# Optimization experiments

Measured on AMD Instinct MI355X. Metric: run time of the kernel, lower is better.

## Reference

```python
import jax, jax.numpy as jnp
import numpy as np

N_NODES = 100000
N_EDGES = 3200000
IN_DIM = 256
HID_DIM = 64
OUT_DIM = 64


def setup_inputs() -> dict:
    key = jax.random.key(0)
    k1, k2, k3, k4, k5, k6 = jax.random.split(key, 6)
    x = jax.random.normal(k1, (N_NODES, IN_DIM), dtype=jnp.float32)
    edge_index = jax.random.randint(k2, (2, N_EDGES), 0, N_NODES, dtype=jnp.int32)
    # Glorot-style init for the two GCNConv layers (PyG default: glorot weight, zero bias)
    W1 = jax.random.normal(k3, (IN_DIM, HID_DIM), dtype=jnp.float32) * (1.0 / np.sqrt(IN_DIM))
    b1 = jnp.zeros((HID_DIM,), dtype=jnp.float32)
    W2 = jax.random.normal(k4, (HID_DIM, OUT_DIM), dtype=jnp.float32) * (1.0 / np.sqrt(HID_DIM))
    b2 = jnp.zeros((OUT_DIM,), dtype=jnp.float32)
    return {"x": x, "edge_index": edge_index, "W1": W1, "b1": b1, "W2": W2, "b2": b2}


def _gcn_conv(x, src, dst, deg_inv_sqrt, W, b, n):
    # PyG GCNConv: h = x W; out_i = sum_j norm_ij * h_j + b, with symmetric norm
    h = x @ W                                   # (n, d_out) small GEMM
    norm = deg_inv_sqrt[src] * deg_inv_sqrt[dst]  # (E+n,)
    msg = norm[:, None] * h[src]                # gather (E+n, d_out)
    agg = jax.ops.segment_sum(msg, dst, num_segments=n)  # scatter-add
    return agg + b


def reference(x, edge_index, W1, b1, W2, b2):
    n = x.shape[0]
    loops = jnp.arange(n, dtype=edge_index.dtype)
    src = jnp.concatenate([edge_index[0], loops])
    dst = jnp.concatenate([edge_index[1], loops])
    # degree on destination (col) with added self-loops, weight 1.0
    deg = jax.ops.segment_sum(jnp.ones_like(dst, dtype=x.dtype), dst, num_segments=n)
    deg_inv_sqrt = jnp.where(deg > 0, jax.lax.rsqrt(deg), 0.0)
    h = jax.nn.relu(_gcn_conv(x, src, dst, deg_inv_sqrt, W1, b1, n))
    return _gcn_conv(h, src, dst, deg_inv_sqrt, W2, b2, n)
```

## Files before the change

kernel.cpp:

```cpp
#include <hip/hip_runtime.h>
#include <cstdint>
#include <cstddef>


#define BIN_SHIFT 7
#define BIN_NODES 128
#define MAX_BINS 1024
#define SUP_SHIFT 11
#define FINE_PER_SUP 16
#define NSUP_MAX 64
#define SCAP 56
#define SRC_BITS 17
#define SRC_MASK ((1 << SRC_BITS) - 1)

typedef unsigned short ushort_t;

typedef __attribute__((ext_vector_type(8))) short bf16x8;
typedef __attribute__((ext_vector_type(4))) float f32x4;

union FragB {
  uint4 u;
  bf16x8 b;
};

__device__ __forceinline__ float4 bfq2f4(uint2 p) {
  float4 r;
  r.x = __uint_as_float(p.x << 16);
  r.y = __uint_as_float(p.x & 0xFFFF0000u);
  r.z = __uint_as_float(p.y << 16);
  r.w = __uint_as_float(p.y & 0xFFFF0000u);
  return r;
}
__device__ __forceinline__ unsigned f2bf(float f) {
  unsigned u = __float_as_uint(f);
  return (u + 0x7FFFu + ((u >> 16) & 1u)) >> 16;
}
__device__ __forceinline__ uint2 f42bfq(float4 f) {
  uint2 r;
  r.x = f2bf(f.x) | (f2bf(f.y) << 16);
  r.y = f2bf(f.z) | (f2bf(f.w) << 16);
  return r;
}

__global__ void zero_int(int* __restrict__ p, int n) {
  int i = blockIdx.x * blockDim.x + threadIdx.x;
  if (i < n) p[i] = 0;
}

__global__ __launch_bounds__(256) void bin_count(const int* __restrict__ dst, int E, int nbins,
                                                 int* __restrict__ binCnt) {
  __shared__ int h[MAX_BINS];
  for (int i = threadIdx.x; i < nbins; i += 256) h[i] = 0;
  __syncthreads();
  int stride = gridDim.x * 256;
  for (int e = blockIdx.x * 256 + threadIdx.x; e < E; e += stride)
    atomicAdd(&h[dst[e] >> BIN_SHIFT], 1);
  __syncthreads();
  for (int i = threadIdx.x; i < nbins; i += 256)
    if (h[i]) atomicAdd(&binCnt[i], h[i]);
}

__global__ __launch_bounds__(256) void bin_scan(const int* __restrict__ binCnt, int nbins, int E,
                                                int* __restrict__ binStart,
                                                int* __restrict__ binCursor,
                                                int* __restrict__ supCursor) {
  __shared__ int s[256];
  int t = threadIdx.x;
  int c[4];
  int sum = 0;
#pragma unroll
  for (int i = 0; i < 4; i++) {
    int idx = t * 4 + i;
    c[i] = (idx < nbins) ? binCnt[idx] : 0;
    sum += c[i];
  }
  int v = sum;
  s[t] = v;
  __syncthreads();
  for (int d = 1; d < 256; d <<= 1) {
    int add = (t >= d) ? s[t - d] : 0;
    __syncthreads();
    s[t] += add;
    __syncthreads();
  }
  int run = s[t] - v;
#pragma unroll
  for (int i = 0; i < 4; i++) {
    int idx = t * 4 + i;
    if (idx < nbins) {
      binStart[idx] = run;
      binCursor[idx] = run;
      if ((idx & (FINE_PER_SUP - 1)) == 0) supCursor[idx >> 4] = run;
      run += c[i];
    }
  }
  if (t == 0) binStart[nbins] = E;
}

__global__ __launch_bounds__(256) void super_fill(const int* __restrict__ src,
                                                  const int* __restrict__ dst, int E, int nsup,
                                                  int* __restrict__ supCursor,
                                                  unsigned* __restrict__ supbuf) {
  __shared__ unsigned stage[NSUP_MAX * SCAP];
  __shared__ int lcnt[NSUP_MAX], lbase[NSUP_MAX], lscan[NSUP_MAX + 1];
  const int tid = threadIdx.x;
  const int t0 = blockIdx.x * 2048;
  const int t1 = min(E, t0 + 2048);

  int dv[8], sv[8];
#pragma unroll
  for (int i = 0; i < 8; i++) {
    int e = t0 + i * 256 + tid;
    if (e < t1) {
      dv[i] = dst[e];
      sv[i] = src[e];
    }
  }
  if (tid < nsup) lcnt[tid] = 0;
  __syncthreads();
#pragma unroll
  for (int i = 0; i < 8; i++) {
    int e = t0 + i * 256 + tid;
    if (e < t1) {
      int d = dv[i];
      int sb = d >> SUP_SHIFT;
      unsigned v = ((unsigned)(d & ((1 << SUP_SHIFT) - 1)) << SRC_BITS) | (unsigned)sv[i];
      int idx = atomicAdd(&lcnt[sb], 1);
      if (idx < SCAP)
        stage[sb * SCAP + idx] = v;
      else {
        int g = atomicAdd(&supCursor[sb], 1);
        supbuf[g] = v;
      }
    }
  }
  __syncthreads();
  if (tid < nsup) {
    int c = min(lcnt[tid], SCAP);
    lcnt[tid] = c;
    lbase[tid] = c ? atomicAdd(&supCursor[tid], c) : 0;
  }
  __syncthreads();
  if (tid < 64) {
    int vv = (tid < nsup) ? lcnt[tid] : 0;
    int ss = vv;
#pragma unroll
    for (int d = 1; d < 64; d <<= 1) {
      int u = __shfl_up(ss, d);
      if (tid >= d) ss += u;
    }
    lscan[tid + 1] = ss;
    if (tid == 0) lscan[0] = 0;
  }
  __syncthreads();
  int total = lscan[nsup];
  for (int j = tid; j < total; j += 256) {
    int lo = 0, hi = nsup;
    while (hi - lo > 1) {
      int mid = (lo + hi) >> 1;
      if (lscan[mid] <= j)
        lo = mid;
      else
        hi = mid;
    }
    int off = j - lscan[lo];
    supbuf[lbase[lo] + off] = stage[lo * SCAP + off];
  }
}

__global__ __launch_bounds__(256) void fine_fill(const unsigned* __restrict__ supbuf,
                                                 const int* __restrict__ binStart, int nbins,
                                                 int* __restrict__ binCursor,
                                                 unsigned* __restrict__ binbuf) {
  __shared__ int lcnt[FINE_PER_SUP], lbase[FINE_PER_SUP];
  int sb = blockIdx.x >> 3, p = blockIdx.x & 7;
  int seg0 = binStart[sb << 4];
  int seg1 = binStart[min((sb + 1) << 4, nbins)];
  int part = (seg1 - seg0 + 7) >> 3;
  int c0 = seg0 + p * part;
  int c1 = min(seg1, c0 + part);
  if (threadIdx.x < FINE_PER_SUP) lcnt[threadIdx.x] = 0;
  __syncthreads();
  for (int i = c0 + threadIdx.x; i < c1; i += 256) atomicAdd(&lcnt[supbuf[i] >> 24], 1);
  __syncthreads();
  if (threadIdx.x < FINE_PER_SUP) {
    int c = lcnt[threadIdx.x];
    lbase[threadIdx.x] = c ? atomicAdd(&binCursor[(sb << 4) + threadIdx.x], c) : 0;
    lcnt[threadIdx.x] = 0;
  }
  __syncthreads();
  for (int i = c0 + threadIdx.x; i < c1; i += 256) {
    unsigned v = supbuf[i];
    unsigned dls = v >> SRC_BITS;
    int f = dls >> BIN_SHIFT;
    unsigned vf = ((dls & (BIN_NODES - 1)) << SRC_BITS) | (v & SRC_MASK);
    int idx = lbase[f] + atomicAdd(&lcnt[f], 1);
    binbuf[idx] = vf;
  }
}

__global__ __launch_bounds__(256) void bin_csr(const unsigned* __restrict__ binbuf,
                                               const int* __restrict__ binStart, int N, int E,
                                               int* __restrict__ rowptr, int* __restrict__ col,
                                               float* __restrict__ dis) {
  __shared__ int cnt[BIN_NODES];
  __shared__ int cur[BIN_NODES];
  __shared__ int pref[BIN_NODES];
  int b = blockIdx.x, t = threadIdx.x;
  int nodeBase = b << BIN_SHIFT;
  if (t < BIN_NODES) cnt[t] = 0;
  __syncthreads();
  int s0 = binStart[b], s1 = binStart[b + 1];
  for (int i = s0 + t; i < s1; i += 256) atomicAdd(&cnt[binbuf[i] >> SRC_BITS], 1);
  __syncthreads();
  int c = 0;
  if (t < BIN_NODES) {
    int node = nodeBase + t;
    if (node < N) {
      c = cnt[t];
      dis[node] = rsqrtf((float)(c + 1));
    }
    pref[t] = c;
  }
  __syncthreads();
  for (int d = 1; d < BIN_NODES; d <<= 1) {
    int add = (t < BIN_NODES && t >= d) ? pref[t - d] : 0;
    __syncthreads();
    if (t < BIN_NODES) pref[t] += add;
    __syncthreads();
  }
  if (t < BIN_NODES) {
    int node = nodeBase + t;
    if (node < N) {
      int ex = s0 + pref[t] - c;
      rowptr[node] = ex;
      cur[t] = ex;
    }
  }
  if (b == 0 && t == 255) rowptr[N] = E;
  __syncthreads();
  for (int i = s0 + t; i < s1; i += 256) {
    unsigned v = binbuf[i];
    int slot = atomicAdd(&cur[v >> SRC_BITS], 1);
    col[slot] = v & SRC_MASK;
  }
}

__global__ __launch_bounds__(256) void wsplit(const float* __restrict__ W1,
                                              const float* __restrict__ W2,
                                              ushort_t* __restrict__ wt1,
                                              ushort_t* __restrict__ wt2) {
  int i = blockIdx.x * 256 + threadIdx.x;
  const float* W;
  ushort_t* wt;
  int K, idx;
  if (i < 256 * 64) {
    W = W1; wt = wt1; K = 256; idx = i;
  } else if (i < 256 * 64 + 64 * 64) {
    W = W2; wt = wt2; K = 64; idx = i - 256 * 64;
  } else
    return;
  int n = idx & 63, k = idx >> 6;
  float f = W[k * 64 + n];
  unsigned u = __float_as_uint(f);
  unsigned hb = u & 0xFFFF0000u;
  float lo = f - __uint_as_float(hb);
  wt[(size_t)n * K + k] = (ushort_t)(u >> 16);
  wt[(size_t)64 * K + (size_t)n * K + k] = (ushort_t)(__float_as_uint(lo) >> 16);
}

__device__ __forceinline__ void split8u(uint4 a, uint4 b, uint4& xh, uint4& xl) {
  unsigned ua[8] = {a.x, a.y, a.z, a.w, b.x, b.y, b.z, b.w};
  unsigned hw[4], lw[4];
#pragma unroll
  for (int p = 0; p < 4; p++) {
    unsigned u0 = ua[2 * p], u1 = ua[2 * p + 1];
    unsigned h0 = u0 & 0xFFFF0000u, h1 = u1 & 0xFFFF0000u;
    float l0 = __uint_as_float(u0) - __uint_as_float(h0);
    float l1 = __uint_as_float(u1) - __uint_as_float(h1);
    hw[p] = (u0 >> 16) | h1;
    lw[p] = (__float_as_uint(l0) >> 16) | (__float_as_uint(l1) & 0xFFFF0000u);
  }
  xh = make_uint4(hw[0], hw[1], hw[2], hw[3]);
  xl = make_uint4(lw[0], lw[1], lw[2], lw[3]);
}

__global__ __launch_bounds__(256, 2) void gemm1_mfma(const float* __restrict__ A,
                                                     const ushort_t* __restrict__ Wt,
                                                     uint2* __restrict__ Cb, int M) {
  constexpr int K = 256;
  __shared__ uint4 xtile[2][4][512];
  const int lane = threadIdx.x & 63;
  const int wv = threadIdx.x >> 6;
  const int l15 = lane & 15;
  const int lq = lane >> 4;
  const int m0 = blockIdx.x * 256 + wv * 64;

  const ushort_t* __restrict__ Wlo = Wt + (size_t)64 * K;

  f32x4 acc[4][4];
#pragma unroll
  for (int a = 0; a < 4; a++)
#pragma unroll
    for (int b = 0; b < 4; b++) acc[a][b] = (f32x4){0.f, 0.f, 0.f, 0.f};

  auto stage_tile = [&](int kt, int buf) {
#pragma unroll
    for (int c = 0; c < 8; c++) {
      int s = c * 64 + lane;
      int r = s >> 3;
      int c4 = (s & 7) ^ (r & 7);
      int nd = m0 + r;
      if (nd >= M) nd = M - 1;
      const float* gp = A + (size_t)nd * K + kt * 32 + c4 * 4;
      __builtin_amdgcn_global_load_lds(
          (const __attribute__((address_space(1))) void*)gp,
          (__attribute__((address_space(3))) void*)&xtile[buf][wv][c * 64], 16, 0, 0);
    }
  };

  stage_tile(0, 0);
  stage_tile(1, 1);
  __builtin_amdgcn_sched_barrier(0);

#pragma unroll
  for (int j = 0; j < 8; j++) {
    FragB w[8];
    {
      const int kb = j * 32 + lq * 8;
#pragma unroll
      for (int nt = 0; nt < 4; nt++) {
        w[nt].u = *(const uint4*)(Wt + (size_t)(nt * 16 + l15) * K + kb);
        w[4 + nt].u = *(const uint4*)(Wlo + (size_t)(nt * 16 + l15) * K + kb);
      }
    }
    __builtin_amdgcn_sched_barrier(0);
    if (j < 7)
      asm volatile("s_waitcnt vmcnt(16)" ::: "memory");
    else
      asm volatile("s_waitcnt vmcnt(8)" ::: "memory");
    __builtin_amdgcn_sched_barrier(0);
    uint4 xa[4][2];
#pragma unroll
    for (int mt = 0; mt < 4; mt++) {
      int mr = mt * 16 + l15;
#pragma unroll
      for (int hh = 0; hh < 2; hh++) {
        int c4 = (lq * 2 + hh) ^ (mr & 7);
        xa[mt][hh] = *(const uint4*)&xtile[j & 1][wv][mr * 8 + c4];
      }
    }
    __builtin_amdgcn_sched_barrier(0);
    asm volatile("s_waitcnt lgkmcnt(0)" ::: "memory");
    __builtin_amdgcn_sched_barrier(0);
    if (j + 2 < 8) stage_tile(j + 2, j & 1);
    __builtin_amdgcn_sched_barrier(0);
#pragma unroll
    for (int mt = 0; mt < 4; mt++) {
      FragB xh, xl;
      split8u(xa[mt][0], xa[mt][1], xh.u, xl.u);
#pragma unroll
      for (int nt = 0; nt < 4; nt++) {
        acc[mt][nt] = __builtin_amdgcn_mfma_f32_16x16x32_bf16(w[nt].b, xh.b, acc[mt][nt], 0, 0, 0);
        acc[mt][nt] = __builtin_amdgcn_mfma_f32_16x16x32_bf16(w[nt].b, xl.b, acc[mt][nt], 0, 0, 0);
      }
#pragma unroll
      for (int nt = 0; nt < 4; nt++) {
        acc[mt][nt] =
            __builtin_amdgcn_mfma_f32_16x16x32_bf16(w[4 + nt].b, xh.b, acc[mt][nt], 0, 0, 0);
      }
    }
  }

#pragma unroll
  for (int mt = 0; mt < 4; mt++) {
    int node = m0 + mt * 16 + l15;
    if (node < M) {
      uint2* cp = Cb + (size_t)node * 16 + lq;
#pragma unroll
      for (int nt = 0; nt < 4; nt++) {
        float4 o = make_float4(acc[mt][nt][0], acc[mt][nt][1], acc[mt][nt][2], acc[mt][nt][3]);
        cp[nt * 4] = f42bfq(o);
      }
    }
  }
}

__global__ __launch_bounds__(256, 3) void gemm2_mfma(const ushort_t* __restrict__ Av,
                                                     const ushort_t* __restrict__ Wt,
                                                     uint2* __restrict__ Cb, int M) {
  constexpr int K = 64;
  constexpr int NT = K / 32;
  const int lane = threadIdx.x & 63;
  const int wv = threadIdx.x >> 6;
  const int l15 = lane & 15;
  const int lq = lane >> 4;
  const int m0 = blockIdx.x * 128 + wv * 32;

  const ushort_t* __restrict__ Wlo = Wt + (size_t)64 * K;

  f32x4 acc[2][4];
#pragma unroll
  for (int a = 0; a < 2; a++)
#pragma unroll
    for (int b = 0; b < 4; b++) acc[a][b] = (f32x4){0.f, 0.f, 0.f, 0.f};

  int node[2], ncl[2];
#pragma unroll
  for (int mt = 0; mt < 2; mt++) {
    node[mt] = m0 + mt * 16 + l15;
    ncl[mt] = node[mt] < M ? node[mt] : (M - 1);
  }

  FragB xa[NT][2], wh[NT][4], wl[NT][4];
#pragma unroll
  for (int t = 0; t < NT; t++)
#pragma unroll
    for (int mt = 0; mt < 2; mt++)
      xa[t][mt].u = *(const uint4*)(Av + (size_t)ncl[mt] * K + t * 32 + lq * 8);
#pragma unroll
  for (int t = 0; t < NT; t++)
#pragma unroll
    for (int nt = 0; nt < 4; nt++) {
      wh[t][nt].u = *(const uint4*)(Wt + (size_t)(nt * 16 + l15) * K + t * 32 + lq * 8);
      wl[t][nt].u = *(const uint4*)(Wlo + (size_t)(nt * 16 + l15) * K + t * 32 + lq * 8);
    }
#pragma unroll
  for (int t = 0; t < NT; t++)
#pragma unroll
    for (int mt = 0; mt < 2; mt++)
#pragma unroll
      for (int nt = 0; nt < 4; nt++) {
        acc[mt][nt] =
            __builtin_amdgcn_mfma_f32_16x16x32_bf16(wh[t][nt].b, xa[t][mt].b, acc[mt][nt], 0, 0, 0);
        acc[mt][nt] =
            __builtin_amdgcn_mfma_f32_16x16x32_bf16(wl[t][nt].b, xa[t][mt].b, acc[mt][nt], 0, 0, 0);
      }

#pragma unroll
  for (int mt = 0; mt < 2; mt++) {
    if (node[mt] < M) {
      uint2* cp = Cb + (size_t)node[mt] * 16 + lq;
#pragma unroll
      for (int nt = 0; nt < 4; nt++) {
        float4 o = make_float4(acc[mt][nt][0], acc[mt][nt][1], acc[mt][nt][2], acc[mt][nt][3]);
        cp[nt * 4] = f42bfq(o);
      }
    }
  }
}

template <bool OUTBF>
__global__ __launch_bounds__(256) void agg_kernel(
    const uint2* __restrict__ h, const int* __restrict__ rowptr, const int* __restrict__ col,
    const float* __restrict__ dis, const float* __restrict__ bias, void* __restrict__ outv,
    int N, int relu) {
  int wid = (blockIdx.x * blockDim.x + threadIdx.x) >> 6;
  if (wid >= N) return;
  int lane = threadIdx.x & 63;
  int sub = lane & 15;
  int quarter = lane >> 4;

  int start = rowptr[wid], end = rowptr[wid + 1];
  float di = dis[wid];

  float4 a0 = make_float4(0.f, 0.f, 0.f, 0.f), a1 = a0, a2 = a0, a3 = a0;
  {
    float4 self = bfq2f4(h[(size_t)wid * 16 + sub]);
    if (quarter == 0) {
      a0.x = di * self.x;
      a0.y = di * self.y;
      a0.z = di * self.z;
      a0.w = di * self.w;
    }
  }

  for (int base = start; base < end; base += 64) {
    int e = base + lane;
    int sj = 0;
    float wj = 0.f;
    if (e < end) {
      sj = col[e];
      wj = dis[sj];
    }
    int cnt = end - base;
    if (cnt > 64) cnt = 64;
    int rounds = (cnt + 3) >> 2;

    uint2 g0, g1, g2, g3;
    float w0, w1, w2, w3;
#define ISSUE(gi, G, W)                                              \
  do {                                                               \
    int _i = (4 * (gi) + quarter) & 63;                              \
    int _s = __shfl(sj, _i);                                         \
    float _w = __shfl(wj, _i);                                       \
    if ((gi) < rounds) {                                             \
      G = h[(size_t)_s * 16 + sub];                                  \
      W = _w;                                                        \
    } else {                                                         \
      G = make_uint2(0u, 0u);                                        \
      W = 0.f;                                                       \
    }                                                                \
  } while (0)

    ISSUE(0, g0, w0);
    ISSUE(1, g1, w1);
    ISSUE(2, g2, w2);
    ISSUE(3, g3, w3);
    int rounds4 = (rounds + 3) & ~3;
    for (int t0 = 0; t0 < rounds4; t0 += 4) {
      {
        float4 gf = bfq2f4(g0);
        a0.x += w0 * gf.x; a0.y += w0 * gf.y; a0.z += w0 * gf.z; a0.w += w0 * gf.w;
      }
      ISSUE(t0 + 4, g0, w0);
      {
        float4 gf = bfq2f4(g1);
        a1.x += w1 * gf.x; a1.y += w1 * gf.y; a1.z += w1 * gf.z; a1.w += w1 * gf.w;
      }
      ISSUE(t0 + 5, g1, w1);
      {
        float4 gf = bfq2f4(g2);
        a2.x += w2 * gf.x; a2.y += w2 * gf.y; a2.z += w2 * gf.z; a2.w += w2 * gf.w;
      }
      ISSUE(t0 + 6, g2, w2);
      {
        float4 gf = bfq2f4(g3);
        a3.x += w3 * gf.x; a3.y += w3 * gf.y; a3.z += w3 * gf.z; a3.w += w3 * gf.w;
      }
      ISSUE(t0 + 7, g3, w3);
    }
#undef ISSUE
  }

  float sx = (a0.x + a1.x) + (a2.x + a3.x);
  float sy = (a0.y + a1.y) + (a2.y + a3.y);
  float sz = (a0.z + a1.z) + (a2.z + a3.z);
  float sw = (a0.w + a1.w) + (a2.w + a3.w);
  sx += __shfl_down(sx, 32); sy += __shfl_down(sy, 32);
  sz += __shfl_down(sz, 32); sw += __shfl_down(sw, 32);
  sx += __shfl_down(sx, 16); sy += __shfl_down(sy, 16);
  sz += __shfl_down(sz, 16); sw += __shfl_down(sw, 16);
  if (quarter == 0) {
    float4 bv = ((const float4*)bias)[sub];
    float4 o = make_float4(di * sx + bv.x, di * sy + bv.y, di * sz + bv.z, di * sw + bv.w);
    if (relu) {
      o.x = fmaxf(o.x, 0.f);
      o.y = fmaxf(o.y, 0.f);
      o.z = fmaxf(o.z, 0.f);
      o.w = fmaxf(o.w, 0.f);
    }
    if (OUTBF)
      ((uint2*)outv)[(size_t)wid * 16 + sub] = f42bfq(o);
    else
      ((float4*)outv)[(size_t)wid * 16 + sub] = o;
  }
}

extern "C" void kernel_launch(void* const* d_in, const int* in_sizes, int n_in,
                              void* d_out, int out_size, void* d_ws, size_t ws_size,
                              hipStream_t stream) {
  const float* x = (const float*)d_in[0];
  const int* ei = (const int*)d_in[1];
  const float* W1 = (const float*)d_in[2];
  const float* b1 = (const float*)d_in[3];
  const float* W2 = (const float*)d_in[4];
  const float* b2 = (const float*)d_in[5];

  const int IN = 256;
  const int E = in_sizes[1] / 2;
  const int N = in_sizes[0] / IN;
  const int* src = ei;
  const int* dst = ei + E;
  const int nbins = (N + BIN_NODES - 1) >> BIN_SHIFT;
  const int nsup = (N + (1 << SUP_SHIFT) - 1) >> SUP_SHIFT;

  char* ws = (char*)d_ws;
  size_t off = 0;
  auto alloc = [&](size_t bytes) -> void* {
    void* p = ws + off;
    off += (bytes + 255) & ~(size_t)255;
    return p;
  };
  int* rowptr = (int*)alloc((size_t)(N + 1) * 4);
  float* dis = (float*)alloc((size_t)N * 4);
  int* binCnt = (int*)alloc(MAX_BINS * 4);
  int* binStart = (int*)alloc((MAX_BINS + 1) * 4);
  int* binCursor = (int*)alloc(MAX_BINS * 4);
  int* supCursor = (int*)alloc(NSUP_MAX * 4);
  int* col = (int*)alloc((size_t)E * 4);
  unsigned* supbuf = (unsigned*)col;
  uint2* out1 = (uint2*)alloc((size_t)N * 64 * 2);
  size_t big = ((size_t)E * 4 > (size_t)N * 128) ? (size_t)E * 4 : (size_t)N * 128;
  unsigned* binbuf = (unsigned*)alloc(big);
  uint2* h = (uint2*)binbuf;
  ushort_t* wt1 = (ushort_t*)alloc((size_t)2 * 64 * 256 * 2);
  ushort_t* wt2 = (ushort_t*)alloc((size_t)2 * 64 * 64 * 2);
  float* outf = (float*)d_out;

  zero_int<<<(nbins + 255) / 256, 256, 0, stream>>>(binCnt, nbins);
  bin_count<<<1024, 256, 0, stream>>>(dst, E, nbins, binCnt);
  bin_scan<<<1, 256, 0, stream>>>(binCnt, nbins, E, binStart, binCursor, supCursor);
  super_fill<<<(E + 2047) / 2048, 256, 0, stream>>>(src, dst, E, nsup, supCursor, supbuf);
  fine_fill<<<nsup * 8, 256, 0, stream>>>(supbuf, binStart, nbins, binCursor, binbuf);
  bin_csr<<<nbins, 256, 0, stream>>>(binbuf, binStart, N, E, rowptr, col, dis);
  wsplit<<<(256 * 64 + 64 * 64 + 255) / 256, 256, 0, stream>>>(W1, W2, wt1, wt2);

  gemm1_mfma<<<(N + 255) / 256, 256, 0, stream>>>(x, wt1, h, N);
  agg_kernel<true><<<(N + 3) / 4, 256, 0, stream>>>(h, rowptr, col, dis, b1, out1, N, 1);
  gemm2_mfma<<<(N + 127) / 128, 256, 0, stream>>>((const ushort_t*)out1, wt2, h, N);
  agg_kernel<false><<<(N + 3) / 4, 256, 0, stream>>>(h, rowptr, col, dis, b2, outf, N, 0);
}
```

Measured before the change: 453.6 us.

## Stage split weights in swizzled LDS for both GEMMs and fuse zeroing into prep

```diff
diff --git a/kernel.cpp b/kernel.cpp
--- a/kernel.cpp
+++ b/kernel.cpp
@@ -42,215 +42,13 @@
   return r;
 }
 
-__global__ void zero_int(int* __restrict__ p, int n) {
-  int i = blockIdx.x * blockDim.x + threadIdx.x;
-  if (i < n) p[i] = 0;
-}
-
-__global__ __launch_bounds__(256) void bin_count(const int* __restrict__ dst, int E, int nbins,
-                                                 int* __restrict__ binCnt) {
-  __shared__ int h[MAX_BINS];
-  for (int i = threadIdx.x; i < nbins; i += 256) h[i] = 0;
-  __syncthreads();
-  int stride = gridDim.x * 256;
-  for (int e = blockIdx.x * 256 + threadIdx.x; e < E; e += stride)
-    atomicAdd(&h[dst[e] >> BIN_SHIFT], 1);
-  __syncthreads();
-  for (int i = threadIdx.x; i < nbins; i += 256)
-    if (h[i]) atomicAdd(&binCnt[i], h[i]);
-}
-
-__global__ __launch_bounds__(256) void bin_scan(const int* __restrict__ binCnt, int nbins, int E,
-                                                int* __restrict__ binStart,
-                                                int* __restrict__ binCursor,
-                                                int* __restrict__ supCursor) {
-  __shared__ int s[256];
-  int t = threadIdx.x;
-  int c[4];
-  int sum = 0;
-#pragma unroll
-  for (int i = 0; i < 4; i++) {
-    int idx = t * 4 + i;
-    c[i] = (idx < nbins) ? binCnt[idx] : 0;
-    sum += c[i];
-  }
-  int v = sum;
-  s[t] = v;
-  __syncthreads();
-  for (int d = 1; d < 256; d <<= 1) {
-    int add = (t >= d) ? s[t - d] : 0;
-    __syncthreads();
-    s[t] += add;
-    __syncthreads();
-  }
-  int run = s[t] - v;
-#pragma unroll
-  for (int i = 0; i < 4; i++) {
-    int idx = t * 4 + i;
-    if (idx < nbins) {
-      binStart[idx] = run;
-      binCursor[idx] = run;
-      if ((idx & (FINE_PER_SUP - 1)) == 0) supCursor[idx >> 4] = run;
-      run += c[i];
-    }
-  }
-  if (t == 0) binStart[nbins] = E;
-}
-
-__global__ __launch_bounds__(256) void super_fill(const int* __restrict__ src,
-                                                  const int* __restrict__ dst, int E, int nsup,
-                                                  int* __restrict__ supCursor,
-                                                  unsigned* __restrict__ supbuf) {
-  __shared__ unsigned stage[NSUP_MAX * SCAP];
-  __shared__ int lcnt[NSUP_MAX], lbase[NSUP_MAX], lscan[NSUP_MAX + 1];
-  const int tid = threadIdx.x;
-  const int t0 = blockIdx.x * 2048;
-  const int t1 = min(E, t0 + 2048);
-
-  int dv[8], sv[8];
-#pragma unroll
-  for (int i = 0; i < 8; i++) {
-    int e = t0 + i * 256 + tid;
-    if (e < t1) {
-      dv[i] = dst[e];
-      sv[i] = src[e];
-    }
-  }
-  if (tid < nsup) lcnt[tid] = 0;
-  __syncthreads();
-#pragma unroll
-  for (int i = 0; i < 8; i++) {
-    int e = t0 + i * 256 + tid;
-    if (e < t1) {
-      int d = dv[i];
-      int sb = d >> SUP_SHIFT;
-      unsigned v = ((unsigned)(d & ((1 << SUP_SHIFT) - 1)) << SRC_BITS) | (unsigned)sv[i];
-      int idx = atomicAdd(&lcnt[sb], 1);
-      if (idx < SCAP)
-        stage[sb * SCAP + idx] = v;
-      else {
-        int g = atomicAdd(&supCursor[sb], 1);
-        supbuf[g] = v;
-      }
-    }
-  }
-  __syncthreads();
-  if (tid < nsup) {
-    int c = min(lcnt[tid], SCAP);
-    lcnt[tid] = c;
-    lbase[tid] = c ? atomicAdd(&supCursor[tid], c) : 0;
-  }
-  __syncthreads();
-  if (tid < 64) {
-    int vv = (tid < nsup) ? lcnt[tid] : 0;
-    int ss = vv;
-#pragma unroll
-    for (int d = 1; d < 64; d <<= 1) {
-      int u = __shfl_up(ss, d);
-      if (tid >= d) ss += u;
-    }
-    lscan[tid + 1] = ss;
-    if (tid == 0) lscan[0] = 0;
-  }
-  __syncthreads();
-  int total = lscan[nsup];
-  for (int j = tid; j < total; j += 256) {
-    int lo = 0, hi = nsup;
-    while (hi - lo > 1) {
-      int mid = (lo + hi) >> 1;
-      if (lscan[mid] <= j)
-        lo = mid;
-      else
-        hi = mid;
-    }
-    int off = j - lscan[lo];
-    supbuf[lbase[lo] + off] = stage[lo * SCAP + off];
-  }
-}
-
-__global__ __launch_bounds__(256) void fine_fill(const unsigned* __restrict__ supbuf,
-                                                 const int* __restrict__ binStart, int nbins,
-                                                 int* __restrict__ binCursor,
-                                                 unsigned* __restrict__ binbuf) {
-  __shared__ int lcnt[FINE_PER_SUP], lbase[FINE_PER_SUP];
-  int sb = blockIdx.x >> 3, p = blockIdx.x & 7;
-  int seg0 = binStart[sb << 4];
-  int seg1 = binStart[min((sb + 1) << 4, nbins)];
-  int part = (seg1 - seg0 + 7) >> 3;
-  int c0 = seg0 + p * part;
-  int c1 = min(seg1, c0 + part);
-  if (threadIdx.x < FINE_PER_SUP) lcnt[threadIdx.x] = 0;
-  __syncthreads();
-  for (int i = c0 + threadIdx.x; i < c1; i += 256) atomicAdd(&lcnt[supbuf[i] >> 24], 1);
-  __syncthreads();
-  if (threadIdx.x < FINE_PER_SUP) {
-    int c = lcnt[threadIdx.x];
-    lbase[threadIdx.x] = c ? atomicAdd(&binCursor[(sb << 4) + threadIdx.x], c) : 0;
-    lcnt[threadIdx.x] = 0;
-  }
-  __syncthreads();
-  for (int i = c0 + threadIdx.x; i < c1; i += 256) {
-    unsigned v = supbuf[i];
-    unsigned dls = v >> SRC_BITS;
-    int f = dls >> BIN_SHIFT;
-    unsigned vf = ((dls & (BIN_NODES - 1)) << SRC_BITS) | (v & SRC_MASK);
-    int idx = lbase[f] + atomicAdd(&lcnt[f], 1);
-    binbuf[idx] = vf;
-  }
-}
-
-__global__ __launch_bounds__(256) void bin_csr(const unsigned* __restrict__ binbuf,
-                                               const int* __restrict__ binStart, int N, int E,
-                                               int* __restrict__ rowptr, int* __restrict__ col,
-                                               float* __restrict__ dis) {
-  __shared__ int cnt[BIN_NODES];
-  __shared__ int cur[BIN_NODES];
-  __shared__ int pref[BIN_NODES];
-  int b = blockIdx.x, t = threadIdx.x;
-  int nodeBase = b << BIN_SHIFT;
-  if (t < BIN_NODES) cnt[t] = 0;
-  __syncthreads();
-  int s0 = binStart[b], s1 = binStart[b + 1];
-  for (int i = s0 + t; i < s1; i += 256) atomicAdd(&cnt[binbuf[i] >> SRC_BITS], 1);
-  __syncthreads();
-  int c = 0;
-  if (t < BIN_NODES) {
-    int node = nodeBase + t;
-    if (node < N) {
-      c = cnt[t];
-      dis[node] = rsqrtf((float)(c + 1));
-    }
-    pref[t] = c;
-  }
-  __syncthreads();
-  for (int d = 1; d < BIN_NODES; d <<= 1) {
-    int add = (t < BIN_NODES && t >= d) ? pref[t - d] : 0;
-    __syncthreads();
-    if (t < BIN_NODES) pref[t] += add;
-    __syncthreads();
-  }
-  if (t < BIN_NODES) {
-    int node = nodeBase + t;
-    if (node < N) {
-      int ex = s0 + pref[t] - c;
-      rowptr[node] = ex;
-      cur[t] = ex;
-    }
-  }
-  if (b == 0 && t == 255) rowptr[N] = E;
-  __syncthreads();
-  for (int i = s0 + t; i < s1; i += 256) {
-    unsigned v = binbuf[i];
-    int slot = atomicAdd(&cur[v >> SRC_BITS], 1);
-    col[slot] = v & SRC_MASK;
-  }
-}
-
-__global__ __launch_bounds__(256) void wsplit(const float* __restrict__ W1,
-                                              const float* __restrict__ W2,
-                                              ushort_t* __restrict__ wt1,
-                                              ushort_t* __restrict__ wt2) {
+__global__ __launch_bounds__(256) void prep(const float* __restrict__ W1,
+                                            const float* __restrict__ W2,
+                                            ushort_t* __restrict__ wt1,
+                                            ushort_t* __restrict__ wt2,
+                                            int* __restrict__ binCnt, int nbins) {
   int i = blockIdx.x * 256 + threadIdx.x;
+  if (i < nbins) binCnt[i] = 0;
   const float* W;
   ushort_t* wt;
   int K, idx;
@@ -269,6 +67,205 @@
   wt[(size_t)64 * K + (size_t)n * K + k] = (ushort_t)(__float_as_uint(lo) >> 16);
 }
 
+__global__ __launch_bounds__(256) void bin_count(const int* __restrict__ dst, int E, int nbins,
+                                                 int* __restrict__ binCnt) {
+  __shared__ int h[MAX_BINS];
+  for (int i = threadIdx.x; i < nbins; i += 256) h[i] = 0;
+  __syncthreads();
+  int stride = gridDim.x * 256;
+  for (int e = blockIdx.x * 256 + threadIdx.x; e < E; e += stride)
+    atomicAdd(&h[dst[e] >> BIN_SHIFT], 1);
+  __syncthreads();
+  for (int i = threadIdx.x; i < nbins; i += 256)
+    if (h[i]) atomicAdd(&binCnt[i], h[i]);
+}
+
+__global__ __launch_bounds__(256) void bin_scan(const int* __restrict__ binCnt, int nbins, int E,
+                                                int* __restrict__ binStart,
+                                                int* __restrict__ binCursor,
+                                                int* __restrict__ supCursor) {
+  __shared__ int s[256];
+  int t = threadIdx.x;
+  int c[4];
+  int sum = 0;
+#pragma unroll
+  for (int i = 0; i < 4; i++) {
+    int idx = t * 4 + i;
+    c[i] = (idx < nbins) ? binCnt[idx] : 0;
+    sum += c[i];
+  }
+  int v = sum;
+  s[t] = v;
+  __syncthreads();
+  for (int d = 1; d < 256; d <<= 1) {
+    int add = (t >= d) ? s[t - d] : 0;
+    __syncthreads();
+    s[t] += add;
+    __syncthreads();
+  }
+  int run = s[t] - v;
+#pragma unroll
+  for (int i = 0; i < 4; i++) {
+    int idx = t * 4 + i;
+    if (idx < nbins) {
+      binStart[idx] = run;
+      binCursor[idx] = run;
+      if ((idx & (FINE_PER_SUP - 1)) == 0) supCursor[idx >> 4] = run;
+      run += c[i];
+    }
+  }
+  if (t == 0) binStart[nbins] = E;
+}
+
+__global__ __launch_bounds__(256) void super_fill(const int* __restrict__ src,
+                                                  const int* __restrict__ dst, int E, int nsup,
+                                                  int* __restrict__ supCursor,
+                                                  unsigned* __restrict__ supbuf) {
+  __shared__ unsigned stage[NSUP_MAX * SCAP];
+  __shared__ int lcnt[NSUP_MAX], lbase[NSUP_MAX], lscan[NSUP_MAX + 1];
+  const int tid = threadIdx.x;
+  const int t0 = blockIdx.x * 2048;
+  const int t1 = min(E, t0 + 2048);
+
+  int dv[8], sv[8];
+#pragma unroll
+  for (int i = 0; i < 8; i++) {
+    int e = t0 + i * 256 + tid;
+    if (e < t1) {
+      dv[i] = dst[e];
+      sv[i] = src[e];
+    }
+  }
+  if (tid < nsup) lcnt[tid] = 0;
+  __syncthreads();
+#pragma unroll
+  for (int i = 0; i < 8; i++) {
+    int e = t0 + i * 256 + tid;
+    if (e < t1) {
+      int d = dv[i];
+      int sb = d >> SUP_SHIFT;
+      unsigned v = ((unsigned)(d & ((1 << SUP_SHIFT) - 1)) << SRC_BITS) | (unsigned)sv[i];
+      int idx = atomicAdd(&lcnt[sb], 1);
+      if (idx < SCAP)
+        stage[sb * SCAP + idx] = v;
+      else {
+        int g = atomicAdd(&supCursor[sb], 1);
+        supbuf[g] = v;
+      }
+    }
+  }
+  __syncthreads();
+  if (tid < nsup) {
+    int c = min(lcnt[tid], SCAP);
+    lcnt[tid] = c;
+    lbase[tid] = c ? atomicAdd(&supCursor[tid], c) : 0;
+  }
+  __syncthreads();
+  if (tid < 64) {
+    int vv = (tid < nsup) ? lcnt[tid] : 0;
+    int ss = vv;
+#pragma unroll
+    for (int d = 1; d < 64; d <<= 1) {
+      int u = __shfl_up(ss, d);
+      if (tid >= d) ss += u;
+    }
+    lscan[tid + 1] = ss;
+    if (tid == 0) lscan[0] = 0;
+  }
+  __syncthreads();
+  int total = lscan[nsup];
+  for (int j = tid; j < total; j += 256) {
+    int lo = 0, hi = nsup;
+    while (hi - lo > 1) {
+      int mid = (lo + hi) >> 1;
+      if (lscan[mid] <= j)
+        lo = mid;
+      else
+        hi = mid;
+    }
+    int off = j - lscan[lo];
+    supbuf[lbase[lo] + off] = stage[lo * SCAP + off];
+  }
+}
+
+__global__ __launch_bounds__(256) void fine_fill(const unsigned* __restrict__ supbuf,
+                                                 const int* __restrict__ binStart, int nbins,
+                                                 int* __restrict__ binCursor,
+                                                 unsigned* __restrict__ binbuf) {
+  __shared__ int lcnt[FINE_PER_SUP], lbase[FINE_PER_SUP];
+  int sb = blockIdx.x >> 3, p = blockIdx.x & 7;
+  int seg0 = binStart[sb << 4];
+  int seg1 = binStart[min((sb + 1) << 4, nbins)];
+  int part = (seg1 - seg0 + 7) >> 3;
+  int c0 = seg0 + p * part;
+  int c1 = min(seg1, c0 + part);
+  if (threadIdx.x < FINE_PER_SUP) lcnt[threadIdx.x] = 0;
+  __syncthreads();
+  for (int i = c0 + threadIdx.x; i < c1; i += 256) atomicAdd(&lcnt[supbuf[i] >> 24], 1);
+  __syncthreads();
+  if (threadIdx.x < FINE_PER_SUP) {
+    int c = lcnt[threadIdx.x];
+    lbase[threadIdx.x] = c ? atomicAdd(&binCursor[(sb << 4) + threadIdx.x], c) : 0;
+    lcnt[threadIdx.x] = 0;
+  }
+  __syncthreads();
+  for (int i = c0 + threadIdx.x; i < c1; i += 256) {
+    unsigned v = supbuf[i];
+    unsigned dls = v >> SRC_BITS;
+    int f = dls >> BIN_SHIFT;
+    unsigned vf = ((dls & (BIN_NODES - 1)) << SRC_BITS) | (v & SRC_MASK);
+    int idx = lbase[f] + atomicAdd(&lcnt[f], 1);
+    binbuf[idx] = vf;
+  }
+}
+
+__global__ __launch_bounds__(256) void bin_csr(const unsigned* __restrict__ binbuf,
+                                               const int* __restrict__ binStart, int N, int E,
+                                               int* __restrict__ rowptr, int* __restrict__ col,
+                                               float* __restrict__ dis) {
+  __shared__ int cnt[BIN_NODES];
+  __shared__ int cur[BIN_NODES];
+  __shared__ int pref[BIN_NODES];
+  int b = blockIdx.x, t = threadIdx.x;
+  int nodeBase = b << BIN_SHIFT;
+  if (t < BIN_NODES) cnt[t] = 0;
+  __syncthreads();
+  int s0 = binStart[b], s1 = binStart[b + 1];
+  for (int i = s0 + t; i < s1; i += 256) atomicAdd(&cnt[binbuf[i] >> SRC_BITS], 1);
+  __syncthreads();
+  int c = 0;
+  if (t < BIN_NODES) {
+    int node = nodeBase + t;
+    if (node < N) {
+      c = cnt[t];
+      dis[node] = rsqrtf((float)(c + 1));
+    }
+    pref[t] = c;
+  }
+  __syncthreads();
+  for (int d = 1; d < BIN_NODES; d <<= 1) {
+    int add = (t < BIN_NODES && t >= d) ? pref[t - d] : 0;
+    __syncthreads();
+    if (t < BIN_NODES) pref[t] += add;
+    __syncthreads();
+  }
+  if (t < BIN_NODES) {
+    int node = nodeBase + t;
+    if (node < N) {
+      int ex = s0 + pref[t] - c;
+      rowptr[node] = ex;
+      cur[t] = ex;
+    }
+  }
+  if (b == 0 && t == 255) rowptr[N] = E;
+  __syncthreads();
+  for (int i = s0 + t; i < s1; i += 256) {
+    unsigned v = binbuf[i];
+    int slot = atomicAdd(&cur[v >> SRC_BITS], 1);
+    col[slot] = v & SRC_MASK;
+  }
+}
+
 __device__ __forceinline__ void split8u(uint4 a, uint4 b, uint4& xh, uint4& xl) {
   unsigned ua[8] = {a.x, a.y, a.z, a.w, b.x, b.y, b.z, b.w};
   unsigned hw[4], lw[4];
@@ -285,18 +282,27 @@
   xl = make_uint4(lw[0], lw[1], lw[2], lw[3]);
 }
 
-__global__ __launch_bounds__(256, 2) void gemm1_mfma(const float* __restrict__ A,
+__global__ __launch_bounds__(256, 1) void gemm1_mfma(const float* __restrict__ A,
                                                      const ushort_t* __restrict__ Wt,
                                                      uint2* __restrict__ Cb, int M) {
   constexpr int K = 256;
   __shared__ uint4 xtile[2][4][512];
+  __shared__ uint4 wlds[4096];
   const int lane = threadIdx.x & 63;
   const int wv = threadIdx.x >> 6;
   const int l15 = lane & 15;
   const int lq = lane >> 4;
   const int m0 = blockIdx.x * 256 + wv * 64;
 
-  const ushort_t* __restrict__ Wlo = Wt + (size_t)64 * K;
+  {
+    const uint4* wg = (const uint4*)Wt;
+    for (int i = threadIdx.x; i < 4096; i += 256) {
+      int row = (i >> 5) & 63;
+      int k = i & 31;
+      wlds[(i & ~31) | (k ^ (row & 7))] = wg[i];
+    }
+  }
+  __syncthreads();
 
   f32x4 acc[4][4];
 #pragma unroll
@@ -326,19 +332,18 @@
 #pragma unroll
   for (int j = 0; j < 8; j++) {
     FragB w[8];
-    {
-      const int kb = j * 32 + lq * 8;
-#pragma unroll
-      for (int nt = 0; nt < 4; nt++) {
-        w[nt].u = *(const uint4*)(Wt + (size_t)(nt * 16 + l15) * K + kb);
-        w[4 + nt].u = *(const uint4*)(Wlo + (size_t)(nt * 16 + l15) * K + kb);
-      }
+#pragma unroll
+    for (int nt = 0; nt < 4; nt++) {
+      int row = nt * 16 + l15;
+      int kc = (j * 4 + lq) ^ (row & 7);
+      w[nt].u = wlds[row * 32 + kc];
+      w[4 + nt].u = wlds[2048 + row * 32 + kc];
     }
     __builtin_amdgcn_sched_barrier(0);
     if (j < 7)
-      asm volatile("s_waitcnt vmcnt(16)" ::: "memory");
+      asm volatile("s_waitcnt vmcnt(8)" ::: "memory");
     else
-      asm volatile("s_waitcnt vmcnt(8)" ::: "memory");
+      asm volatile("s_waitcnt vmcnt(0)" ::: "memory");
     __builtin_amdgcn_sched_barrier(0);
     uint4 xa[4][2];
 #pragma unroll
@@ -391,13 +396,22 @@
                                                      uint2* __restrict__ Cb, int M) {
   constexpr int K = 64;
   constexpr int NT = K / 32;
+  __shared__ uint4 w2[1024];
   const int lane = threadIdx.x & 63;
   const int wv = threadIdx.x >> 6;
   const int l15 = lane & 15;
   const int lq = lane >> 4;
   const int m0 = blockIdx.x * 128 + wv * 32;
 
-  const ushort_t* __restrict__ Wlo = Wt + (size_t)64 * K;
+  {
+    const uint4* wg = (const uint4*)Wt;
+    for (int i = threadIdx.x; i < 1024; i += 256) {
+      int row = (i >> 3) & 63;
+      int k = i & 7;
+      w2[(i & ~7) | (k ^ (row & 7))] = wg[i];
+    }
+  }
+  __syncthreads();
 
   f32x4 acc[2][4];
 #pragma unroll
@@ -412,30 +426,33 @@
     ncl[mt] = node[mt] < M ? node[mt] : (M - 1);
   }
 
-  FragB xa[NT][2], wh[NT][4], wl[NT][4];
+  FragB xa[NT][2];
 #pragma unroll
   for (int t = 0; t < NT; t++)
 #pragma unroll
     for (int mt = 0; mt < 2; mt++)
       xa[t][mt].u = *(const uint4*)(Av + (size_t)ncl[mt] * K + t * 32 + lq * 8);
-#pragma unroll
-  for (int t = 0; t < NT; t++)
+
+#pragma unroll
+  for (int t = 0; t < NT; t++) {
+    FragB wh[4], wl[4];
 #pragma unroll
     for (int nt = 0; nt < 4; nt++) {
-      wh[t][nt].u = *(const uint4*)(Wt + (size_t)(nt * 16 + l15) * K + t * 32 + lq * 8);
-      wl[t][nt].u = *(const uint4*)(Wlo + (size_t)(nt * 16 + l15) * K + t * 32 + lq * 8);
-    }
-#pragma unroll
-  for (int t = 0; t < NT; t++)
+      int row = nt * 16 + l15;
+      int kc = (t * 4 + lq) ^ (row & 7);
+      wh[nt].u = w2[row * 8 + kc];
+      wl[nt].u = w2[512 + row * 8 + kc];
+    }
 #pragma unroll
     for (int mt = 0; mt < 2; mt++)
 #pragma unroll
       for (int nt = 0; nt < 4; nt++) {
         acc[mt][nt] =
-            __builtin_amdgcn_mfma_f32_16x16x32_bf16(wh[t][nt].b, xa[t][mt].b, acc[mt][nt], 0, 0, 0);
+            __builtin_amdgcn_mfma_f32_16x16x32_bf16(wh[nt].b, xa[t][mt].b, acc[mt][nt], 0, 0, 0);
         acc[mt][nt] =
-            __builtin_amdgcn_mfma_f32_16x16x32_bf16(wl[t][nt].b, xa[t][mt].b, acc[mt][nt], 0, 0, 0);
-      }
+            __builtin_amdgcn_mfma_f32_16x16x32_bf16(wl[nt].b, xa[t][mt].b, acc[mt][nt], 0, 0, 0);
+      }
+  }
 
 #pragma unroll
   for (int mt = 0; mt < 2; mt++) {
@@ -598,13 +615,12 @@
   ushort_t* wt2 = (ushort_t*)alloc((size_t)2 * 64 * 64 * 2);
   float* outf = (float*)d_out;
 
-  zero_int<<<(nbins + 255) / 256, 256, 0, stream>>>(binCnt, nbins);
+  prep<<<(256 * 64 + 64 * 64 + 255) / 256, 256, 0, stream>>>(W1, W2, wt1, wt2, binCnt, nbins);
   bin_count<<<1024, 256, 0, stream>>>(dst, E, nbins, binCnt);
   bin_scan<<<1, 256, 0, stream>>>(binCnt, nbins, E, binStart, binCursor, supCursor);
   super_fill<<<(E + 2047) / 2048, 256, 0, stream>>>(src, dst, E, nsup, supCursor, supbuf);
   fine_fill<<<nsup * 8, 256, 0, stream>>>(supbuf, binStart, nbins, binCursor, binbuf);
   bin_csr<<<nbins, 256, 0, stream>>>(binbuf, binStart, N, E, rowptr, col, dis);
-  wsplit<<<(256 * 64 + 64 * 64 + 255) / 256, 256, 0, stream>>>(W1, W2, wt1, wt2);
 
   gemm1_mfma<<<(N + 255) / 256, 256, 0, stream>>>(x, wt1, h, N);
   agg_kernel<true><<<(N + 3) / 4, 256, 0, stream>>>(h, rowptr, col, dis, b1, out1, N, 1);
```

Result: no change. 447.4 us (-1.4%).
